# Kernel tuning notes

Hardware: AMD Instinct MI355X
Metric: run time of the kernel (lower is better)

The kernel has to match this reference:

```python
import jax, jax.numpy as jnp
import numpy as np
from jax import lax

B_BLK = 16   # block size B
N_Z = 64     # latent dim


def setup_inputs() -> dict:
    key = jax.random.key(0)
    ks = jax.random.split(key, 6)
    in_ch, out_ch = 256, 256
    L = (out_ch // B_BLK) * (in_ch // B_BLK)  # 256 latent codes
    x = jax.random.normal(ks[0], (32, in_ch, 64, 64), dtype=jnp.float32)
    z = jax.random.normal(ks[1], (L, N_Z), dtype=jnp.float32)
    W1 = jax.random.normal(ks[2], (B_BLK, N_Z, N_Z), dtype=jnp.float32) * 0.1
    B1 = jax.random.normal(ks[3], (B_BLK, N_Z), dtype=jnp.float32) * 0.1
    W2 = jax.random.normal(ks[4], (B_BLK, B_BLK * 9, N_Z), dtype=jnp.float32) * 0.1
    B2 = jax.random.normal(ks[5], (B_BLK, B_BLK * 9), dtype=jnp.float32) * 0.1
    return {"x": x, "z": z, "W1": W1, "B1": B1, "W2": W2, "B2": B2}


def _aggregate_weight(z, W1, B1, W2, B2, out_ch, in_ch):
    # hypertype='separate', batched over all L = (out_ch//B)*(in_ch//B) blocks.
    # per block: a = W1 @ z + B1 -> (B, N_z); K = W2 @ a[...,None] + B2 -> (B, B*9)
    a = jnp.einsum('bdn,ln->lbd', W1, z) + B1            # (L, B, N_z)
    K = jnp.einsum('bkd,lbd->lbk', W2, a) + B2           # (L, B, B*9)
    ob, ib = out_ch // B_BLK, in_ch // B_BLK
    K = K.reshape(ob, ib, B_BLK, B_BLK, 3, 3)            # (o_blk, i_blk, b1, b2, 3, 3)
    # torch: K.reshape(B,B,3,3).permute(1,0,2,3) => weight_block[p,q] = K[q,p]
    # then cat over i_blk on dim 1 (in), over o_blk on dim 0 (out)
    w = K.transpose(0, 3, 1, 2, 4, 5)                    # (o_blk, b2, i_blk, b1, 3, 3)
    return w.reshape(out_ch, in_ch, 3, 3)


def reference(x, z, W1, B1, W2, B2):
    out_ch, in_ch = 256, 256
    weight = _aggregate_weight(z, W1, B1, W2, B2, out_ch, in_ch)
    # F.conv2d(x, weight, bias=None, stride=1, padding=kernel_size//2=1)
    return lax.conv_general_dilated(
        x, weight,
        window_strides=(1, 1),
        padding=[(1, 1), (1, 1)],
        dimension_numbers=('NCHW', 'OIHW', 'NCHW'))
```

## Files before the change

kernel.cpp:

```cpp
#include <hip/hip_runtime.h>

typedef unsigned short u16;
typedef unsigned int u32;
typedef __attribute__((ext_vector_type(8))) short short8;
typedef __attribute__((ext_vector_type(4))) float f32x4;

__device__ __forceinline__ u16 f2bf(float f) {
    u32 u = __float_as_uint(f);
    return (u16)((u + 0x7FFFu + ((u >> 16) & 1u)) >> 16);
}

__global__ __launch_bounds__(256) void nchw2nhwc(const float* __restrict__ x,
                                                 u16* __restrict__ xb) {
    __shared__ float tile[64][65];
    const int b   = blockIdx.x;
    const int n   = b >> 8;
    const int icb = (b >> 6) & 3;
    const int pxb = b & 63;
    const int ic0 = icb * 64, px0 = pxb * 64;

    const int g = threadIdx.x >> 6, lx = threadIdx.x & 63;
    const float* src = x + (size_t)(n * 256 + ic0) * 4096 + px0 + lx;
#pragma unroll
    for (int r = 0; r < 16; ++r) {
        int row = g * 16 + r;
        tile[row][lx] = src[(size_t)row * 4096];
    }
    __syncthreads();
    const int tp = threadIdx.x & 31, pz = threadIdx.x >> 5;
    u16* dst = xb + ((size_t)(n * 4096) + px0) * 256 + ic0 + tp * 2;
#pragma unroll
    for (int r = 0; r < 8; ++r) {
        int p = pz * 8 + r;
        u32 pv = ((u32)f2bf(tile[tp * 2 + 1][p]) << 16) | f2bf(tile[tp * 2][p]);
        *(u32*)(dst + (size_t)p * 256) = pv;
    }
}

__global__ __launch_bounds__(256) void wgen(const float* __restrict__ z,
                                            const float* __restrict__ W1,
                                            const float* __restrict__ B1,
                                            const float* __restrict__ W2,
                                            const float* __restrict__ B2,
                                            u16* __restrict__ wb) {
    __shared__ float zl[64];
    __shared__ float aL[1024];
    const int l = blockIdx.x;
    const int tid = threadIdx.x;
    if (tid < 64) zl[tid] = z[l * 64 + tid];
    __syncthreads();
#pragma unroll
    for (int i = 0; i < 4; ++i) {
        int idx = i * 256 + tid;
        const float* wrow = W1 + (size_t)idx * 64;
        float s = B1[idx];
        for (int nn = 0; nn < 64; ++nn) s += wrow[nn] * zl[nn];
        aL[idx] = s;
    }
    __syncthreads();
    const int b1 = tid >> 4, b2 = tid & 15;
    const int ob = l >> 4, ib = l & 15;
    const int ic = ib * 16 + b1;
    const int oc = ob * 16 + b2;
    const size_t wbase = (size_t)oc * 2304 + (size_t)(ic >> 5) * 288 + (ic & 31);
    const float* arow = aL + b1 * 64;
#pragma unroll
    for (int tap = 0; tap < 9; ++tap) {
        int kk = b2 * 9 + tap;
        const float* w2row = W2 + (size_t)(b1 * 144 + kk) * 64;
        float s = B2[b1 * 144 + kk];
        for (int d = 0; d < 64; ++d) s += w2row[d] * arow[d];
        wb[wbase + tap * 32] = f2bf(s);
    }
}

__global__ __launch_bounds__(256) void conv_mfma(const u16* __restrict__ xb,
                                                 const u16* __restrict__ wb,
                                                 float* __restrict__ out) {
    __shared__ __align__(16) u16 As[128 * 32];
    __shared__ __align__(16) u16 Bs[128 * 32];

    const int tid = threadIdx.x;
    const int bid = blockIdx.x;
    const int mt = bid & 1;
    const int nt = bid >> 1;
    const int n = nt >> 5;
    const int pimg = (nt & 31) << 7;
    const int oc0 = mt << 7;

    const int lane = tid & 63;
    const int wave = tid >> 6;
    const int wm = (wave >> 1) & 1, wn = wave & 1;
    const int lr = lane & 15, lq = lane >> 4;

    const int qa = tid, qb = tid + 256;
    const int r0 = qa >> 2, c0 = qa & 3;
    const int r1 = qb >> 2, c1 = qb & 3;

    const u16* aw0 = wb + (size_t)(oc0 + r0) * 2304 + c0 * 8;
    const u16* aw1 = wb + (size_t)(oc0 + r1) * 2304 + c1 * 8;
    u16* asw0 = As + r0 * 32 + c0 * 8;
    u16* asw1 = As + r1 * 32 + c1 * 8;

    const int po0 = pimg + r0, po1 = pimg + r1;
    const int ho0 = po0 >> 6, wo0 = po0 & 63;
    const int ho1 = po1 >> 6, wo1 = po1 & 63;
    const u16* bx0 = xb + ((size_t)n * 4096 + po0) * 256 + c0 * 8;
    const u16* bx1 = xb + ((size_t)n * 4096 + po1) * 256 + c1 * 8;
    u16* bsw0 = Bs + r0 * 32 + c0 * 8;
    u16* bsw1 = Bs + r1 * 32 + c1 * 8;

    f32x4 acc[4][4];
    const f32x4 z4 = {0.f, 0.f, 0.f, 0.f};
#pragma unroll
    for (int i = 0; i < 4; ++i)
#pragma unroll
        for (int j = 0; j < 4; ++j) acc[i][j] = z4;

    int icb = 0, tap = 0;
    for (int kt = 0; kt < 72; ++kt) {
        const int dh = tap / 3 - 1, dw = tap % 3 - 1;
        const int goff = (dh * 64 + dw) * 256 + icb * 32;
        const int aoffk = kt * 32;

        uint4 av0 = *(const uint4*)(aw0 + aoffk);
        uint4 av1 = *(const uint4*)(aw1 + aoffk);
        uint4 bv0 = {0, 0, 0, 0}, bv1 = {0, 0, 0, 0};
        {
            int hi = ho0 + dh, wi = wo0 + dw;
            if ((unsigned)hi < 64u && (unsigned)wi < 64u)
                bv0 = *(const uint4*)(bx0 + goff);
        }
        {
            int hi = ho1 + dh, wi = wo1 + dw;
            if ((unsigned)hi < 64u && (unsigned)wi < 64u)
                bv1 = *(const uint4*)(bx1 + goff);
        }
        *(uint4*)asw0 = av0;
        *(uint4*)asw1 = av1;
        *(uint4*)bsw0 = bv0;
        *(uint4*)bsw1 = bv1;
        __syncthreads();

        short8 af[4], bf[4];
#pragma unroll
        for (int i = 0; i < 4; ++i) {
            af[i] = *(const short8*)(As + (wm * 64 + i * 16 + lr) * 32 + lq * 8);
            bf[i] = *(const short8*)(Bs + (wn * 64 + i * 16 + lr) * 32 + lq * 8);
        }
#pragma unroll
        for (int i = 0; i < 4; ++i)
#pragma unroll
            for (int j = 0; j < 4; ++j)
                acc[i][j] = __builtin_amdgcn_mfma_f32_16x16x32_bf16(
                    af[i], bf[j], acc[i][j], 0, 0, 0);
        __syncthreads();
        if (++tap == 9) { tap = 0; ++icb; }
    }

    const size_t outn = (size_t)n * 256 * 4096;
#pragma unroll
    for (int i = 0; i < 4; ++i) {
        int ocb = oc0 + wm * 64 + i * 16 + lq * 4;
#pragma unroll
        for (int j = 0; j < 4; ++j) {
            int po = pimg + wn * 64 + j * 16 + lr;
            float* op = out + outn + (size_t)ocb * 4096 + po;
#pragma unroll
            for (int r = 0; r < 4; ++r) op[(size_t)r * 4096] = acc[i][j][r];
        }
    }
}

extern "C" void kernel_launch(void* const* d_in, const int* in_sizes, int n_in,
                              void* d_out, int out_size, void* d_ws, size_t ws_size,
                              hipStream_t stream) {
    const float* x  = (const float*)d_in[0];
    const float* z  = (const float*)d_in[1];
    const float* W1 = (const float*)d_in[2];
    const float* B1 = (const float*)d_in[3];
    const float* W2 = (const float*)d_in[4];
    const float* B2 = (const float*)d_in[5];
    float* out = (float*)d_out;

    u16* xb = (u16*)d_ws;
    u16* wb = xb + (size_t)32 * 4096 * 256;
    const size_t need = ((size_t)32 * 4096 * 256 + (size_t)256 * 2304) * 2;
    if (ws_size < need) return;

    nchw2nhwc<<<dim3(8192), dim3(256), 0, stream>>>(x, xb);
    wgen<<<dim3(256), dim3(256), 0, stream>>>(z, W1, B1, W2, B2, wb);
    conv_mfma<<<dim3(2048), dim3(256), 0, stream>>>(xb, wb, out);
}
```

Baseline: 462.5 us.

## Use direct global-to-LDS loads in conv, vectorize transpose, remap blocks per XCD

```diff
diff --git a/kernel.cpp b/kernel.cpp
--- a/kernel.cpp
+++ b/kernel.cpp
@@ -4,36 +4,51 @@
 typedef unsigned int u32;
 typedef __attribute__((ext_vector_type(8))) short short8;
 typedef __attribute__((ext_vector_type(4))) float f32x4;
+typedef __attribute__((ext_vector_type(4))) unsigned short u16x4;
 
 __device__ __forceinline__ u16 f2bf(float f) {
     u32 u = __float_as_uint(f);
     return (u16)((u + 0x7FFFu + ((u >> 16) & 1u)) >> 16);
 }
 
+__device__ __forceinline__ void gl2lds16(const u16* g, u16* l) {
+    __builtin_amdgcn_global_load_lds(
+        (const __attribute__((address_space(1))) u32*)g,
+        (__attribute__((address_space(3))) u32*)l, 16, 0, 0);
+}
+
 __global__ __launch_bounds__(256) void nchw2nhwc(const float* __restrict__ x,
                                                  u16* __restrict__ xb) {
-    __shared__ float tile[64][65];
+    __shared__ u16 t[64 * 72];
     const int b   = blockIdx.x;
     const int n   = b >> 8;
     const int icb = (b >> 6) & 3;
     const int pxb = b & 63;
     const int ic0 = icb * 64, px0 = pxb * 64;
-
-    const int g = threadIdx.x >> 6, lx = threadIdx.x & 63;
-    const float* src = x + (size_t)(n * 256 + ic0) * 4096 + px0 + lx;
-#pragma unroll
-    for (int r = 0; r < 16; ++r) {
-        int row = g * 16 + r;
-        tile[row][lx] = src[(size_t)row * 4096];
+    const int tid = threadIdx.x;
+
+    const int icq = tid >> 4;
+    const int px4 = (tid & 15) * 4;
+    const float* src = x + (size_t)(n * 256 + ic0 + icq * 4) * 4096 + px0 + px4;
+    f32x4 v[4];
+#pragma unroll
+    for (int rr = 0; rr < 4; ++rr) v[rr] = *(const f32x4*)(src + (size_t)rr * 4096);
+#pragma unroll
+    for (int j = 0; j < 4; ++j) {
+        u16x4 p;
+        p.x = f2bf(v[0][j]); p.y = f2bf(v[1][j]);
+        p.z = f2bf(v[2][j]); p.w = f2bf(v[3][j]);
+        *(u16x4*)(t + (px4 + j) * 72 + icq * 4) = p;
     }
     __syncthreads();
-    const int tp = threadIdx.x & 31, pz = threadIdx.x >> 5;
-    u16* dst = xb + ((size_t)(n * 4096) + px0) * 256 + ic0 + tp * 2;
-#pragma unroll
-    for (int r = 0; r < 8; ++r) {
-        int p = pz * 8 + r;
-        u32 pv = ((u32)f2bf(tile[tp * 2 + 1][p]) << 16) | f2bf(tile[tp * 2][p]);
-        *(u32*)(dst + (size_t)p * 256) = pv;
+
+    const int c = tid & 7, pxr = tid >> 3;
+    u16* dstb = xb + ((size_t)(n * 4096) + px0) * 256 + ic0 + c * 8;
+#pragma unroll
+    for (int h = 0; h < 2; ++h) {
+        int px = h * 32 + pxr;
+        uint4 val = *(const uint4*)(t + px * 72 + c * 8);
+        *(uint4*)(dstb + (size_t)px * 256) = val;
     }
 }
 
@@ -42,11 +57,13 @@
                                             const float* __restrict__ B1,
                                             const float* __restrict__ W2,
                                             const float* __restrict__ B2,
-                                            u16* __restrict__ wb) {
+                                            u16* __restrict__ wb,
+                                            u16* __restrict__ zpad) {
     __shared__ float zl[64];
     __shared__ float aL[1024];
     const int l = blockIdx.x;
     const int tid = threadIdx.x;
+    if (l == 0 && tid < 32) zpad[tid] = 0;
     if (tid < 64) zl[tid] = z[l * 64 + tid];
     __syncthreads();
 #pragma unroll
@@ -76,14 +93,16 @@
 
 __global__ __launch_bounds__(256) void conv_mfma(const u16* __restrict__ xb,
                                                  const u16* __restrict__ wb,
+                                                 const u16* __restrict__ zpad,
                                                  float* __restrict__ out) {
     __shared__ __align__(16) u16 As[128 * 32];
     __shared__ __align__(16) u16 Bs[128 * 32];
 
     const int tid = threadIdx.x;
     const int bid = blockIdx.x;
-    const int mt = bid & 1;
-    const int nt = bid >> 1;
+    const int xcd = bid & 7, rest = bid >> 3;
+    const int mt = rest & 1, grp = rest >> 1;
+    const int nt = grp * 8 + xcd;
     const int n = nt >> 5;
     const int pimg = (nt & 31) << 7;
     const int oc0 = mt << 7;
@@ -93,22 +112,29 @@
     const int wm = (wave >> 1) & 1, wn = wave & 1;
     const int lr = lane & 15, lq = lane >> 4;
 
-    const int qa = tid, qb = tid + 256;
-    const int r0 = qa >> 2, c0 = qa & 3;
-    const int r1 = qb >> 2, c1 = qb & 3;
+    const int r0 = tid >> 2, c0 = tid & 3;
+    const int q1 = tid + 256, r1 = q1 >> 2, c1 = q1 & 3;
 
     const u16* aw0 = wb + (size_t)(oc0 + r0) * 2304 + c0 * 8;
     const u16* aw1 = wb + (size_t)(oc0 + r1) * 2304 + c1 * 8;
-    u16* asw0 = As + r0 * 32 + c0 * 8;
-    u16* asw1 = As + r1 * 32 + c1 * 8;
+    u16* al0 = As + tid * 8;
+    u16* al1 = As + (tid + 256) * 8;
+    u16* bl0 = Bs + tid * 8;
+    u16* bl1 = Bs + (tid + 256) * 8;
 
     const int po0 = pimg + r0, po1 = pimg + r1;
     const int ho0 = po0 >> 6, wo0 = po0 & 63;
     const int ho1 = po1 >> 6, wo1 = po1 & 63;
-    const u16* bx0 = xb + ((size_t)n * 4096 + po0) * 256 + c0 * 8;
-    const u16* bx1 = xb + ((size_t)n * 4096 + po1) * 256 + c1 * 8;
-    u16* bsw0 = Bs + r0 * 32 + c0 * 8;
-    u16* bsw1 = Bs + r1 * 32 + c1 * 8;
+    const u16* bx0 = xb + ((size_t)(n * 4096) + po0) * 256 + c0 * 8;
+    const u16* bx1 = xb + ((size_t)(n * 4096) + po1) * 256 + c1 * 8;
+
+    bool m0[9], m1[9];
+#pragma unroll
+    for (int tap = 0; tap < 9; ++tap) {
+        const int dh = tap / 3 - 1, dw = tap % 3 - 1;
+        m0[tap] = ((unsigned)(ho0 + dh) < 64u) & ((unsigned)(wo0 + dw) < 64u);
+        m1[tap] = ((unsigned)(ho1 + dh) < 64u) & ((unsigned)(wo1 + dw) < 64u);
+    }
 
     f32x4 acc[4][4];
     const f32x4 z4 = {0.f, 0.f, 0.f, 0.f};
@@ -117,45 +143,33 @@
 #pragma unroll
         for (int j = 0; j < 4; ++j) acc[i][j] = z4;
 
-    int icb = 0, tap = 0;
-    for (int kt = 0; kt < 72; ++kt) {
-        const int dh = tap / 3 - 1, dw = tap % 3 - 1;
-        const int goff = (dh * 64 + dw) * 256 + icb * 32;
-        const int aoffk = kt * 32;
-
-        uint4 av0 = *(const uint4*)(aw0 + aoffk);
-        uint4 av1 = *(const uint4*)(aw1 + aoffk);
-        uint4 bv0 = {0, 0, 0, 0}, bv1 = {0, 0, 0, 0};
-        {
-            int hi = ho0 + dh, wi = wo0 + dw;
-            if ((unsigned)hi < 64u && (unsigned)wi < 64u)
-                bv0 = *(const uint4*)(bx0 + goff);
+    for (int icb = 0; icb < 8; ++icb) {
+#pragma unroll
+        for (int tap = 0; tap < 9; ++tap) {
+            const int dh = tap / 3 - 1, dw = tap % 3 - 1;
+            const int toff = (dh * 64 + dw) * 256 + icb * 32;
+            const int koff = (icb * 9 + tap) * 32;
+
+            gl2lds16(aw0 + koff, al0);
+            gl2lds16(aw1 + koff, al1);
+            gl2lds16(m0[tap] ? bx0 + toff : zpad, bl0);
+            gl2lds16(m1[tap] ? bx1 + toff : zpad, bl1);
+            __syncthreads();
+
+            short8 af[4], bfr[4];
+#pragma unroll
+            for (int i = 0; i < 4; ++i) {
+                af[i]  = *(const short8*)(As + (wm * 64 + i * 16 + lr) * 32 + lq * 8);
+                bfr[i] = *(const short8*)(Bs + (wn * 64 + i * 16 + lr) * 32 + lq * 8);
+            }
+#pragma unroll
+            for (int i = 0; i < 4; ++i)
+#pragma unroll
+                for (int j = 0; j < 4; ++j)
+                    acc[i][j] = __builtin_amdgcn_mfma_f32_16x16x32_bf16(
+                        af[i], bfr[j], acc[i][j], 0, 0, 0);
+            __syncthreads();
         }
-        {
-            int hi = ho1 + dh, wi = wo1 + dw;
-            if ((unsigned)hi < 64u && (unsigned)wi < 64u)
-                bv1 = *(const uint4*)(bx1 + goff);
-        }
-        *(uint4*)asw0 = av0;
-        *(uint4*)asw1 = av1;
-        *(uint4*)bsw0 = bv0;
-        *(uint4*)bsw1 = bv1;
-        __syncthreads();
-
-        short8 af[4], bf[4];
-#pragma unroll
-        for (int i = 0; i < 4; ++i) {
-            af[i] = *(const short8*)(As + (wm * 64 + i * 16 + lr) * 32 + lq * 8);
-            bf[i] = *(const short8*)(Bs + (wn * 64 + i * 16 + lr) * 32 + lq * 8);
-        }
-#pragma unroll
-        for (int i = 0; i < 4; ++i)
-#pragma unroll
-            for (int j = 0; j < 4; ++j)
-                acc[i][j] = __builtin_amdgcn_mfma_f32_16x16x32_bf16(
-                    af[i], bf[j], acc[i][j], 0, 0, 0);
-        __syncthreads();
-        if (++tap == 9) { tap = 0; ++icb; }
     }
 
     const size_t outn = (size_t)n * 256 * 4096;
@@ -185,10 +199,11 @@
 
     u16* xb = (u16*)d_ws;
     u16* wb = xb + (size_t)32 * 4096 * 256;
-    const size_t need = ((size_t)32 * 4096 * 256 + (size_t)256 * 2304) * 2;
+    u16* zp = wb + (size_t)256 * 2304;
+    const size_t need = ((size_t)32 * 4096 * 256 + (size_t)256 * 2304 + 32) * 2;
     if (ws_size < need) return;
 
     nchw2nhwc<<<dim3(8192), dim3(256), 0, stream>>>(x, xb);
-    wgen<<<dim3(256), dim3(256), 0, stream>>>(z, W1, B1, W2, B2, wb);
-    conv_mfma<<<dim3(2048), dim3(256), 0, stream>>>(xb, wb, out);
-}
+    wgen<<<dim3(256), dim3(256), 0, stream>>>(z, W1, B1, W2, B2, wb, zp);
+    conv_mfma<<<dim3(2048), dim3(256), 0, stream>>>(xb, wb, zp, out);
+}
```

Measured after the change: 469.3 us. Within noise of the previous version (+1.5%).
